# Optimization experiments

Hardware: AMD Instinct MI355X
Metric: run time of the kernel (lower is better)

Reference implementation:

```python
import jax, jax.numpy as jnp
import numpy as np

HEADS = 8
BN_EPS = 1e-5

def _bn(x2d, g, b):
    # torch BatchNorm1d in training mode: biased batch stats
    mu = x2d.mean(0)
    var = x2d.var(0)
    return (x2d - mu) * jax.lax.rsqrt(var + BN_EPS) * g + b

def _window_indices(H):
    # exclusive-end box coordinates, in the exact order of the torch loop
    m = H // 2
    r0, r1, c0, c1 = [], [], [], []
    for i in range(1, m + 1):
        wins = [(m - i, m + i + 1, m - i, m + i + 1),  # full square
                (m - i, m + 1,     m - i, m + i + 1),  # top half
                (m,     m + i + 1, m - i, m + i + 1),  # bottom half
                (m - i, m + i + 1, m - i, m + 1),      # left half
                (m - i, m + i + 1, m,     m + i + 1)]  # right half
        for a, b, c, d in wins:
            r0.append(a); r1.append(b); c0.append(c); c1.append(d)
    r0 = np.array(r0); r1 = np.array(r1); c0 = np.array(c0); c1 = np.array(c1)
    counts = ((r1 - r0) * (c1 - c0)).astype(np.float32)
    return r0, r1, c0, c1, counts

def _box_sums(P, r0, r1, c0, c1):
    # P: padded 2D prefix sum [B, C, H+1, H+1]; returns [B, C, K]
    return P[:, :, r1, c1] - P[:, :, r0, c1] - P[:, :, r1, c0] + P[:, :, r0, c0]

def _integral(img):
    return jnp.pad(jnp.cumsum(jnp.cumsum(img, axis=2), axis=3), ((0, 0), (0, 0), (1, 0), (1, 0)))

def setup_inputs() -> dict:
    key = jax.random.key(0)
    ks = jax.random.split(key, 8)
    B, Cin, H = 64, 512, 31
    C = 512  # heads * base_dim
    x = jax.random.normal(ks[0], (B, Cin, H, H), dtype=jnp.float32)
    w_v = jax.random.normal(ks[1], (Cin, C), dtype=jnp.float32) * 0.02
    w_k = jax.random.normal(ks[2], (Cin, C), dtype=jnp.float32) * 0.02
    w_fc = jax.random.normal(ks[3], (Cin + C, 512), dtype=jnp.float32) * 0.02
    z = lambda n: jnp.zeros((n,), jnp.float32)
    o = lambda n: jnp.ones((n,), jnp.float32)
    return {"x": x,
            "w_v": w_v, "b_v": z(C), "g_vn": o(C), "b_vn": z(C),
            "w_k": w_k, "b_k": z(C), "g_kn": o(C), "b_kn": z(C),
            "w_fc": w_fc, "b_fc": z(512), "g_fcn": o(512), "b_fcn": z(512)}

def reference(x, w_v, b_v, g_vn, b_vn, w_k, b_k, g_kn, b_kn, w_fc, b_fc, g_fcn, b_fcn):
    B, Cin, H, W = x.shape
    N = H * W
    C = w_v.shape[1]
    d = C // HEADS
    m = H // 2
    xt = x.reshape(B, Cin, N).transpose(0, 2, 1)       # [B, N, Cin]
    x0 = xt[:, N // 2, :]                              # [B, Cin] center pixel feature
    flat = xt.reshape(B * N, Cin)
    v = jax.nn.relu(_bn(flat @ w_v + b_v, g_vn, b_vn))
    v = v.reshape(B, N, C).transpose(0, 2, 1).reshape(B, C, H, H)
    k = _bn(flat @ w_k + b_k, g_kn, b_kn).reshape(B, N, HEADS, d).transpose(0, 2, 1, 3)  # [B,h,N,d]
    q = k[:, :, N // 2, :]                             # [B, h, d]
    attn = jax.nn.softmax(jnp.einsum('bhd,bhnd->bhn', q, k) * (d ** -0.5), axis=-1)      # [B,h,N]
    attn_full = jnp.broadcast_to(attn[:, :, None, :], (B, HEADS, d, N)).reshape(B, C, H, H)
    xw = attn_full * v                                 # attn-weighted values [B,C,H,H]
    eps = 1e-16
    r0, r1, c0, c1, counts = _window_indices(H)
    Px = _integral(xw)
    Pa = _integral(attn_full)
    mx = _box_sums(Px, r0, r1, c0, c1) / counts        # window means of xw   [B,C,K]
    ma = _box_sums(Pa, r0, r1, c0, c1) / counts        # window means of attn [B,C,K]
    y_win = (mx / (ma + eps)).transpose(0, 2, 1)       # [B, K, C]
    y = jnp.concatenate([xw[:, :, m, m][:, None, :], y_win], axis=1)  # [B, n, C]
    # F.normalize(p=2, dim=2)
    y = y / jnp.maximum(jnp.linalg.norm(y, axis=2, keepdims=True), 1e-12)
    n = y.shape[1]
    yy = jnp.concatenate([jnp.broadcast_to(x0[:, None, :], (B, n, Cin)), y], axis=-1)
    out = jax.nn.relu(_bn(yy.reshape(B * n, Cin + C) @ w_fc + b_fc, g_fcn, b_fcn))
    return out.reshape(B, n, -1)
```

## Files before the change

kernel.cpp:

```cpp
#include <hip/hip_runtime.h>
#include <stdint.h>

#define DEV __device__ __forceinline__

typedef __bf16 bf16x8 __attribute__((ext_vector_type(8)));
typedef unsigned short u16x8 __attribute__((ext_vector_type(8)));
typedef uint32_t u32x4 __attribute__((ext_vector_type(4)));
typedef float f32x4 __attribute__((ext_vector_type(4)));

#define NS 1024

DEV uint16_t f2bf(float f) {
    union { float f; uint32_t u; } v; v.f = f;
    uint32_t r = v.u + 0x7fffu + ((v.u >> 16) & 1u);
    return (uint16_t)(r >> 16);
}
DEV float bf2f(uint16_t h) {
    union { uint32_t u; float f; } v; v.u = ((uint32_t)h) << 16;
    return v.f;
}

#if __has_builtin(__builtin_amdgcn_cvt_pk_bf16_f32)
typedef __bf16 bf16x2 __attribute__((ext_vector_type(2)));
DEV uint32_t pk2bf(float lo, float hi) {
    bf16x2 r = __builtin_amdgcn_cvt_pk_bf16_f32(lo, hi);
    return __builtin_bit_cast(uint32_t, r);
}
#else
DEV uint32_t pk2bf(float lo, float hi) {
    return (uint32_t)f2bf(lo) | ((uint32_t)f2bf(hi) << 16);
}
#endif

DEV float scan32(float v, int lane) {
    #pragma unroll
    for (int d = 1; d < 32; d <<= 1) {
        float o = __shfl_up(v, d, 32);
        if (lane >= d) v += o;
    }
    return v;
}

DEV void win_idx(int w, int& r0, int& r1, int& c0, int& c1) {
    int i = w / 5 + 1, t = w % 5;
    const int m = 15;
    switch (t) {
        case 0: r0 = m - i; r1 = m + i + 1; c0 = m - i; c1 = m + i + 1; break;
        case 1: r0 = m - i; r1 = m + 1;     c0 = m - i; c1 = m + i + 1; break;
        case 2: r0 = m;     r1 = m + i + 1; c0 = m - i; c1 = m + i + 1; break;
        case 3: r0 = m - i; r1 = m + i + 1; c0 = m - i; c1 = m + 1;     break;
        default:r0 = m - i; r1 = m + i + 1; c0 = m;     c1 = m + i + 1; break;
    }
}

#if __has_builtin(__builtin_amdgcn_global_load_lds)
DEV void async16(const uint16_t* g, uint16_t* l) {
    __builtin_amdgcn_global_load_lds(
        (const __attribute__((address_space(1))) uint32_t*)g,
        (__attribute__((address_space(3))) uint32_t*)l, 16, 0, 0);
}
#else
DEV void async16(const uint16_t* g, uint16_t* l) {
    *(u16x8*)l = *(const u16x8*)g;
}
#endif

__global__ void k_convert_x(const float* __restrict__ x, uint16_t* __restrict__ xbt) {
    __shared__ float tile[32][33];
    int b = blockIdx.z;
    int n0 = blockIdx.x * 32;
    int c0 = blockIdx.y * 32;
    int tx = threadIdx.x, ty = threadIdx.y;
    #pragma unroll
    for (int i = 0; i < 4; ++i) {
        int c = c0 + ty + 8 * i;
        int n = n0 + tx;
        float v = 0.f;
        if (n < 961) v = x[((size_t)b * 512 + c) * 961 + n];
        tile[ty + 8 * i][tx] = v;
    }
    __syncthreads();
    int idx = ty * 32 + tx;
    int c4 = (idx & 7) * 4;
    int nl = idx >> 3;
    int n = n0 + nl;
    ushort4 val;
    val.x = f2bf(tile[c4 + 0][nl]);
    val.y = f2bf(tile[c4 + 1][nl]);
    val.z = f2bf(tile[c4 + 2][nl]);
    val.w = f2bf(tile[c4 + 3][nl]);
    *(ushort4*)&xbt[((size_t)b * NS + n) * 512 + c0 + c4] = val;
}

__global__ void k_convert_w(const float* __restrict__ wv, const float* __restrict__ wk,
                            const float* __restrict__ wfc,
                            uint16_t* __restrict__ wvkt, uint16_t* __restrict__ wfct,
                            uint16_t* __restrict__ wfrag) {
    int idx = blockIdx.x * 256 + threadIdx.x;
    if (idx < 524288) {
        int j = idx >> 9, k = idx & 511;
        float v = (j < 512) ? wv[(size_t)k * 512 + j] : wk[(size_t)k * 512 + (j - 512)];
        wvkt[idx] = f2bf(v);
    } else if (idx < 1048576) {
        int t = idx - 524288;
        int j = t >> 10, k = t & 1023;
        wfct[t] = f2bf(wfc[(size_t)k * 512 + j]);
    } else {
        int t = idx - 1048576;
        int e = t & 7;
        int lane = (t >> 3) & 63;
        int kt = (t >> 9) & 31;
        int mt = t >> 14;
        int m = mt * 16 + (lane & 15);
        int k = kt * 32 + (lane >> 4) * 8 + e;
        uint16_t out = 0;
        if (m < 75 && k < 961) {
            int r = k / 31, cc = k - r * 31;
            int r0, r1, c0, c1;
            win_idx(m, r0, r1, c0, c1);
            if (r >= r0 && r < r1 && cc >= c0 && cc < c1) out = 0x3f80;
        }
        wfrag[t] = out;
    }
}

template<int K, int EPI>
__global__ __launch_bounds__(256, 4)
void k_gemm(const uint16_t* __restrict__ A, const uint16_t* __restrict__ Bt,
            uint16_t* __restrict__ out_v, uint16_t* __restrict__ out_k,
            float* __restrict__ out_f,
            float* __restrict__ colsum, float* __restrict__ colsq)
{
    __shared__ __align__(16) uint16_t sbuf[16384];
    __shared__ float sStat[256];
    uint16_t* sA0 = sbuf;
    uint16_t* sA1 = sbuf + 4096;
    uint16_t* sB0 = sbuf + 8192;
    uint16_t* sB1 = sbuf + 12288;

    const int tid = threadIdx.x;
    const int wave = tid >> 6, lane = tid & 63;
    const int quad = lane >> 4, l16 = lane & 15;
    int m0, j0;
    if constexpr (EPI == 0) {
        int lin = blockIdx.x;
        int xcd = lin & 7, rest = lin >> 3;
        int jb = rest & 7, mhi = rest >> 3;
        m0 = (mhi * 8 + xcd) * 128; j0 = jb * 128;
    } else {
        m0 = blockIdx.y * 128; j0 = blockIdx.x * 128;
    }
    const int wm = wave >> 1, wj = wave & 1;

    const f32x4 fzero = {0.f, 0.f, 0.f, 0.f};
    f32x4 acc[4][4];
    #pragma unroll
    for (int i = 0; i < 4; ++i)
        #pragma unroll
        for (int j = 0; j < 4; ++j) acc[i][j] = fzero;

    const int c0 = tid;
    const int mA0 = c0 >> 2, kq0 = c0 & 3;
    const int c1 = tid + 256;
    const int mA1 = c1 >> 2, kq1 = c1 & 3;

    const int KT = K / 64;
    for (int kt = 0; kt < KT; ++kt) {
        const uint16_t* Ak = A + (size_t)m0 * K + kt * 64;
        const uint16_t* Bk = Bt + (size_t)j0 * K + kt * 64;
        async16(Ak + (size_t)mA0 * K + kq0 * 8,      &sA0[c0 * 8]);
        async16(Ak + (size_t)mA1 * K + kq1 * 8,      &sA0[c1 * 8]);
        async16(Ak + (size_t)mA0 * K + 32 + kq0 * 8, &sA1[c0 * 8]);
        async16(Ak + (size_t)mA1 * K + 32 + kq1 * 8, &sA1[c1 * 8]);
        async16(Bk + (size_t)mA0 * K + kq0 * 8,      &sB0[c0 * 8]);
        async16(Bk + (size_t)mA1 * K + kq1 * 8,      &sB0[c1 * 8]);
        async16(Bk + (size_t)mA0 * K + 32 + kq0 * 8, &sB1[c0 * 8]);
        async16(Bk + (size_t)mA1 * K + 32 + kq1 * 8, &sB1[c1 * 8]);
        __syncthreads();
        #pragma unroll
        for (int p = 0; p < 2; ++p) {
            const uint16_t* pA = p ? sA1 : sA0;
            const uint16_t* pB = p ? sB1 : sB0;
            bf16x8 af[4], bfr[4];
            #pragma unroll
            for (int i = 0; i < 4; ++i) {
                int m = wm * 64 + i * 16 + l16;
                u16x8 r = *(const u16x8*)&pA[m * 32 + quad * 8];
                af[i] = __builtin_bit_cast(bf16x8, r);
            }
            #pragma unroll
            for (int j = 0; j < 4; ++j) {
                int jj = wj * 64 + j * 16 + l16;
                u16x8 r = *(const u16x8*)&pB[jj * 32 + quad * 8];
                bfr[j] = __builtin_bit_cast(bf16x8, r);
            }
            #pragma unroll
            for (int i = 0; i < 4; ++i)
                #pragma unroll
                for (int j = 0; j < 4; ++j)
                    acc[i][j] = __builtin_amdgcn_mfma_f32_16x16x32_bf16(af[i], bfr[j], acc[i][j], 0, 0, 0);
        }
        __syncthreads();
    }

    sStat[tid] = 0.f;
    __syncthreads();

    #pragma unroll
    for (int j = 0; j < 4; ++j) {
        const int col_local = wj * 64 + j * 16 + l16;
        float ls = 0.f, lq = 0.f;
        #pragma unroll
        for (int i = 0; i < 4; ++i) {
            #pragma unroll
            for (int reg = 0; reg < 4; ++reg) {
                const float val = acc[i][j][reg];
                ls += val; lq += val * val;
                if constexpr (EPI == 1) {
                    const int r = m0 + wm * 64 + i * 16 + quad * 4 + reg;
                    out_f[(size_t)r * 512 + (j0 + col_local)] = val;
                }
            }
        }
        ls += __shfl_xor(ls, 16); lq += __shfl_xor(lq, 16);
        ls += __shfl_xor(ls, 32); lq += __shfl_xor(lq, 32);
        if (quad == 0) {
            atomicAdd(&sStat[col_local], ls);
            atomicAdd(&sStat[128 + col_local], lq);
        }
    }
    __syncthreads();
    if (tid < 128) atomicAdd(&colsum[j0 + tid], sStat[tid]);
    else           atomicAdd(&colsq[j0 + (tid & 127)], sStat[tid]);

    if constexpr (EPI == 0) {
        #pragma unroll
        for (int ch = 0; ch < 2; ++ch) {
            if (wj == ch) {
                #pragma unroll
                for (int j = 0; j < 4; ++j) {
                    const int c = j * 16 + l16;
                    #pragma unroll
                    for (int i = 0; i < 4; ++i) {
                        const int rloc = wm * 64 + i * 16 + quad * 4;
                        uint2 pp;
                        pp.x = pk2bf(acc[i][j][0], acc[i][j][1]);
                        pp.y = pk2bf(acc[i][j][2], acc[i][j][3]);
                        *(uint2*)&sbuf[c * 136 + rloc] = pp;
                    }
                }
            }
            __syncthreads();
            const int jg = j0 + ch * 64;
            uint16_t* const outp = (jg < 512) ? out_v : out_k;
            const int jbase = (jg < 512) ? jg : jg - 512;
            #pragma unroll
            for (int s = 0; s < 8; ++s) {
                const int chunk = tid + 256 * s;
                const int c = chunk >> 5, q = chunk & 31;
                uint2 val = *(const uint2*)&sbuf[c * 136 + q * 4];
                const int r = m0 + q * 4;
                const unsigned bb_ = (unsigned)r >> 10;
                const unsigned nn = (unsigned)r & 1023u;
                *(uint2*)&outp[((size_t)bb_ * 512 + jbase + c) * NS + nn] = val;
            }
            __syncthreads();
        }
    }
}

__global__ __launch_bounds__(256, 4)
void k_attnwin(const uint16_t* __restrict__ kraw, const uint16_t* __restrict__ vraw,
               const uint16_t* __restrict__ wfrag,
               const float* __restrict__ colsum, const float* __restrict__ colsq,
               const float* __restrict__ g_kn, const float* __restrict__ b_kn,
               const float* __restrict__ g_vn, const float* __restrict__ b_vn,
               float* __restrict__ y)
{
    __shared__ float qa[64];
    __shared__ float va[64], vb[64];
    __shared__ float atv[992];
    __shared__ __align__(16) uint16_t attb[1024];
    __shared__ float maw_s[80];
    __shared__ float cnt_s[80];
    __shared__ float red[4];
    __shared__ float s_qb, s_bmax, s_inv;

    const int bh = blockIdx.x;
    const int b = bh >> 3, h = bh & 7;
    const int tid = threadIdx.x;
    const int lane = tid & 63, wave = tid >> 6;
    const int quad = lane >> 4, l16 = lane & 15;
    constexpr float invM = 1.f / 61504.f;

    if (tid < 64) {
        int c = h * 64 + tid;
        float mean = colsum[512 + c] * invM;
        float q_ = colsq[512 + c] * invM;
        float a = g_kn[c] * rsqrtf(q_ - mean * mean + 1e-5f);
        float bb = b_kn[c] - mean * a;
        float kr = bf2f(kraw[((size_t)b * 512 + c) * NS + 480]);
        float qv = kr * a + bb;
        qa[tid] = qv * a;
        float qb = qv * bb;
        #pragma unroll
        for (int off = 32; off; off >>= 1) qb += __shfl_down(qb, off);
        if (tid == 0) s_qb = qb;
    } else if (tid < 128) {
        int t = tid - 64;
        int c = h * 64 + t;
        float mean = colsum[c] * invM;
        float q_ = colsq[c] * invM;
        float a = g_vn[c] * rsqrtf(q_ - mean * mean + 1e-5f);
        va[t] = a;
        vb[t] = b_vn[c] - mean * a;
    }
    __syncthreads();

    const int n4 = tid * 4;
    float lg[4];
    float lmax = -1e30f;
    {
        const uint16_t* kp = kraw + ((size_t)b * 512 + h * 64) * NS + n4;
        float a0 = 0.f, a1 = 0.f, a2 = 0.f, a3 = 0.f;
        if (n4 < 961) {
            #pragma unroll 16
            for (int dd = 0; dd < 64; ++dd) {
                uint2 kk = *(const uint2*)(kp + (size_t)dd * NS);
                u16x8 kk4 = {};
                kk4[0] = (uint16_t)(kk.x & 0xffffu);
                kk4[1] = (uint16_t)(kk.x >> 16);
                kk4[2] = (uint16_t)(kk.y & 0xffffu);
                kk4[3] = (uint16_t)(kk.y >> 16);
                float q = qa[dd];
                a0 += q * bf2f(kk4[0]);
                a1 += q * bf2f(kk4[1]);
                a2 += q * bf2f(kk4[2]);
                a3 += q * bf2f(kk4[3]);
            }
        }
        lg[0] = a0; lg[1] = a1; lg[2] = a2; lg[3] = a3;
        #pragma unroll
        for (int i = 0; i < 4; ++i) {
            lg[i] = (lg[i] + s_qb) * 0.125f;
            if (n4 + i < 961) lmax = fmaxf(lmax, lg[i]);
        }
    }
    #pragma unroll
    for (int off = 32; off; off >>= 1) lmax = fmaxf(lmax, __shfl_xor(lmax, off));
    if (lane == 0) red[wave] = lmax;
    __syncthreads();
    if (tid == 0) s_bmax = fmaxf(fmaxf(red[0], red[1]), fmaxf(red[2], red[3]));
    __syncthreads();
    float lsum = 0.f;
    #pragma unroll
    for (int i = 0; i < 4; ++i) {
        float e = (n4 + i < 961) ? __expf(lg[i] - s_bmax) : 0.f;
        lg[i] = e;
        lsum += e;
    }
    #pragma unroll
    for (int off = 32; off; off >>= 1) lsum += __shfl_xor(lsum, off);
    if (lane == 0) red[wave] = lsum;
    __syncthreads();
    if (tid == 0) s_inv = 1.f / (red[0] + red[1] + red[2] + red[3]);
    __syncthreads();
    {
        uint2 pk;
        float w0 = (n4 + 0 < 961) ? lg[0] * s_inv : 0.f;
        float w1 = (n4 + 1 < 961) ? lg[1] * s_inv : 0.f;
        float w2 = (n4 + 2 < 961) ? lg[2] * s_inv : 0.f;
        float w3 = (n4 + 3 < 961) ? lg[3] * s_inv : 0.f;
        pk.x = pk2bf(w0, w1);
        pk.y = pk2bf(w2, w3);
        *(uint2*)&attb[n4] = pk;
        #pragma unroll
        for (int i = 0; i < 4; ++i)
            if (n4 + i < 961) atv[n4 + i] = lg[i] * s_inv;
    }
    __syncthreads();

    if (tid < 64) {
        float vv = bf2f(vraw[((size_t)(b * 512 + h * 64 + tid)) * NS + 480]);
        y[(size_t)b * 76 * 512 + h * 64 + tid] = fmaxf(vv * va[tid] + vb[tid], 0.f) * atv[480];
    }
    __syncthreads();

    {
        int col = tid & 31, r8 = tid >> 5;
        #pragma unroll
        for (int p = 0; p < 4; ++p) {
            int row = p * 8 + r8;
            bool on = (row < 31) && (col < 31);
            float v = on ? atv[row * 31 + col] : 0.f;
            v = scan32(v, col);
            if (on) atv[row * 31 + col] = v;
        }
    }
    __syncthreads();
    {
        int r = tid & 31, c8 = tid >> 5;
        #pragma unroll
        for (int p = 0; p < 4; ++p) {
            int cc = p * 8 + c8;
            bool on = (cc < 31) && (r < 31);
            float v = on ? atv[r * 31 + cc] : 0.f;
            v = scan32(v, r);
            if (on) atv[r * 31 + cc] = v;
        }
    }
    __syncthreads();
    if (tid < 75) {
        int r0, r1, c0, c1;
        win_idx(tid, r0, r1, c0, c1);
        auto S = [&](int r, int c) -> float { return (r < 0 || c < 0) ? 0.f : atv[r * 31 + c]; };
        float box = S(r1 - 1, c1 - 1) - S(r0 - 1, c1 - 1) - S(r1 - 1, c0 - 1) + S(r0 - 1, c0 - 1);
        float cnt = (float)((r1 - r0) * (c1 - c0));
        cnt_s[tid] = cnt;
        maw_s[tid] = box / cnt;
    }
    __syncthreads();

    {
        const int cl = wave * 16 + l16;
        const float a_bn = va[cl], b_bn = vb[cl];
        const uint16_t* vp = vraw + ((size_t)(b * 512 + h * 64 + cl)) * NS + quad * 8;
        f32x4 acc5[5];
        const f32x4 fz = {0.f, 0.f, 0.f, 0.f};
        #pragma unroll
        for (int mt = 0; mt < 5; ++mt) acc5[mt] = fz;
        for (int kt = 0; kt < 31; ++kt) {
            u16x8 vv = *(const u16x8*)(vp + kt * 32);
            u16x8 aa = *(const u16x8*)&attb[kt * 32 + quad * 8];
            u32x4 bwu;
            #pragma unroll
            for (int e = 0; e < 4; ++e) {
                float x0 = fmaxf(bf2f(vv[2 * e]) * a_bn + b_bn, 0.f) * bf2f(aa[2 * e]);
                float x1 = fmaxf(bf2f(vv[2 * e + 1]) * a_bn + b_bn, 0.f) * bf2f(aa[2 * e + 1]);
                bwu[e] = pk2bf(x0, x1);
            }
            bf16x8 bfr = __builtin_bit_cast(bf16x8, bwu);
            #pragma unroll
            for (int mt = 0; mt < 5; ++mt) {
                u16x8 wf = *(const u16x8*)&wfrag[(((mt * 32 + kt) * 64 + lane)) * 8];
                acc5[mt] = __builtin_amdgcn_mfma_f32_16x16x32_bf16(
                    __builtin_bit_cast(bf16x8, wf), bfr, acc5[mt], 0, 0, 0);
            }
        }
        const int cg = h * 64 + cl;
        #pragma unroll
        for (int mt = 0; mt < 5; ++mt) {
            #pragma unroll
            for (int reg = 0; reg < 4; ++reg) {
                int w = mt * 16 + quad * 4 + reg;
                if (w < 75) {
                    float mx = acc5[mt][reg] / cnt_s[w];
                    y[((size_t)b * 76 + 1 + w) * 512 + cg] = mx / (maw_s[w] + 1e-16f);
                }
            }
        }
    }
}

__global__ void k_build_yy(const float* __restrict__ y, const uint16_t* __restrict__ xbt,
                           uint16_t* __restrict__ yy)
{
    __shared__ float red[4];
    int row = blockIdx.x;
    int b = row / 76;
    int tid = threadIdx.x;
    const float* yp = y + (size_t)row * 512;
    float v0 = yp[tid], v1 = yp[tid + 256];
    float ss = v0 * v0 + v1 * v1;
    for (int off = 32; off; off >>= 1) ss += __shfl_xor(ss, off);
    if ((tid & 63) == 0) red[tid >> 6] = ss;
    __syncthreads();
    float tot = red[0] + red[1] + red[2] + red[3];
    float inv = 1.f / fmaxf(sqrtf(tot), 1e-12f);
    uint16_t* op = yy + (size_t)row * 1024;
    const uint16_t* x0p = xbt + ((size_t)b * NS + 480) * 512;
    op[tid]           = x0p[tid];
    op[tid + 256]     = x0p[tid + 256];
    op[512 + tid]       = f2bf(v0 * inv);
    op[512 + tid + 256] = f2bf(v1 * inv);
}

__global__ void k_fcout(const float* __restrict__ fcraw,
                        const float* __restrict__ colsum, const float* __restrict__ colsq,
                        const float* __restrict__ g, const float* __restrict__ be,
                        float* __restrict__ out)
{
    size_t idx = (size_t)blockIdx.x * 256 + threadIdx.x;
    if (idx < (size_t)4864 * 512) {
        int j = (int)(idx & 511);
        constexpr float invM = 1.f / 4864.f;
        float mean = colsum[j] * invM;
        float q_ = colsq[j] * invM;
        float a = g[j] * rsqrtf(q_ - mean * mean + 1e-5f);
        float bb = be[j] - mean * a;
        out[idx] = fmaxf(fcraw[idx] * a + bb, 0.f);
    }
}

extern "C" void kernel_launch(void* const* d_in, const int* in_sizes, int n_in,
                              void* d_out, int out_size, void* d_ws, size_t ws_size,
                              hipStream_t stream)
{
    (void)in_sizes; (void)n_in; (void)out_size; (void)ws_size;
    const float* x    = (const float*)d_in[0];
    const float* w_v  = (const float*)d_in[1];
    const float* g_vn = (const float*)d_in[3];
    const float* b_vn = (const float*)d_in[4];
    const float* w_k  = (const float*)d_in[5];
    const float* g_kn = (const float*)d_in[7];
    const float* b_kn = (const float*)d_in[8];
    const float* w_fc = (const float*)d_in[9];
    const float* g_fcn = (const float*)d_in[11];
    const float* b_fcn = (const float*)d_in[12];
    float* out = (float*)d_out;

    char* base = (char*)d_ws;
    size_t off = 0;
    auto alloc = [&](size_t bytes) -> void* {
        void* p = base + off;
        off += (bytes + 255) & ~(size_t)255;
        return p;
    };
    uint16_t* xbt  = (uint16_t*)alloc((size_t)64 * NS * 512 * 2);
    uint16_t* wvkt = (uint16_t*)alloc((size_t)1024 * 512 * 2);
    uint16_t* wfct = (uint16_t*)alloc((size_t)512 * 1024 * 2);
    uint16_t* wfrag = (uint16_t*)alloc((size_t)5 * 32 * 64 * 8 * 2);
    uint16_t* vraw = (uint16_t*)alloc((size_t)64 * 512 * NS * 2);
    uint16_t* kraw = (uint16_t*)alloc((size_t)64 * 512 * NS * 2);
    float* stats   = (float*)alloc(3072 * 4);
    float* y       = (float*)alloc((size_t)64 * 76 * 512 * 4);
    uint16_t* yy   = (uint16_t*)alloc((size_t)4864 * 1024 * 2);
    float* fcraw   = (float*)alloc((size_t)4864 * 512 * 4);

    hipMemsetAsync(stats, 0, 3072 * 4, stream);
    k_convert_x<<<dim3(32, 16, 64), dim3(32, 8), 0, stream>>>(x, xbt);
    k_convert_w<<<4416, 256, 0, stream>>>(w_v, w_k, w_fc, wvkt, wfct, wfrag);

    k_gemm<512, 0><<<4096, 256, 0, stream>>>(xbt, wvkt, vraw, kraw, nullptr,
                                             stats, stats + 1024);

    k_attnwin<<<512, 256, 0, stream>>>(kraw, vraw, wfrag, stats, stats + 1024,
                                       g_kn, b_kn, g_vn, b_vn, y);
    k_build_yy<<<4864, 256, 0, stream>>>(y, xbt, yy);

    k_gemm<1024, 1><<<dim3(4, 38), 256, 0, stream>>>(yy, wfct, nullptr, nullptr, fcraw,
                                                     stats + 2048, stats + 2560);
    k_fcout<<<9728, 256, 0, stream>>>(fcraw, stats + 2048, stats + 2560, g_fcn, b_fcn, out);
}
```

Baseline: 423.6 us.

## Fuse fp32-to-bf16 transpose of x into the V/K projection GEMM A-load

Removes the separate k_convert_x kernel and its bf16 transposed copy of x. The QKV GEMM now reads fp32 x directly along the spatial dimension, converts to bf16 in registers and writes the transposed tile into padded LDS. This saves one full write and read pass of a 64x1024x512 bf16 buffer and one launch. The cost is a synchronous global load path in place of async LDS loads, and each wave reading 8 channel rows, which could lower load efficiency. build_yy now reads x0 from x directly.

```diff
diff --git a/kernel.cpp b/kernel.cpp
--- a/kernel.cpp
+++ b/kernel.cpp
@@ -64,33 +64,6 @@
     *(u16x8*)l = *(const u16x8*)g;
 }
 #endif
-
-__global__ void k_convert_x(const float* __restrict__ x, uint16_t* __restrict__ xbt) {
-    __shared__ float tile[32][33];
-    int b = blockIdx.z;
-    int n0 = blockIdx.x * 32;
-    int c0 = blockIdx.y * 32;
-    int tx = threadIdx.x, ty = threadIdx.y;
-    #pragma unroll
-    for (int i = 0; i < 4; ++i) {
-        int c = c0 + ty + 8 * i;
-        int n = n0 + tx;
-        float v = 0.f;
-        if (n < 961) v = x[((size_t)b * 512 + c) * 961 + n];
-        tile[ty + 8 * i][tx] = v;
-    }
-    __syncthreads();
-    int idx = ty * 32 + tx;
-    int c4 = (idx & 7) * 4;
-    int nl = idx >> 3;
-    int n = n0 + nl;
-    ushort4 val;
-    val.x = f2bf(tile[c4 + 0][nl]);
-    val.y = f2bf(tile[c4 + 1][nl]);
-    val.z = f2bf(tile[c4 + 2][nl]);
-    val.w = f2bf(tile[c4 + 3][nl]);
-    *(ushort4*)&xbt[((size_t)b * NS + n) * 512 + c0 + c4] = val;
-}
 
 __global__ void k_convert_w(const float* __restrict__ wv, const float* __restrict__ wk,
                             const float* __restrict__ wfc,
@@ -124,13 +97,156 @@
     }
 }
 
-template<int K, int EPI>
 __global__ __launch_bounds__(256, 4)
-void k_gemm(const uint16_t* __restrict__ A, const uint16_t* __restrict__ Bt,
-            uint16_t* __restrict__ out_v, uint16_t* __restrict__ out_k,
-            float* __restrict__ out_f,
-            float* __restrict__ colsum, float* __restrict__ colsq)
+void k_gemmx(const float* __restrict__ x, const uint16_t* __restrict__ Bt,
+             uint16_t* __restrict__ out_v, uint16_t* __restrict__ out_k,
+             float* __restrict__ colsum, float* __restrict__ colsq)
 {
+    constexpr int K = 512;
+    __shared__ __align__(16) uint16_t sA[2][128 * 40];
+    __shared__ __align__(16) uint16_t sB[2][128 * 32];
+    __shared__ float sStat[256];
+
+    const int tid = threadIdx.x;
+    const int wave = tid >> 6, lane = tid & 63;
+    const int quad = lane >> 4, l16 = lane & 15;
+    int lin = blockIdx.x;
+    int xcd = lin & 7, rest = lin >> 3;
+    int jb = rest & 7, mhi = rest >> 3;
+    const int mb = mhi * 8 + xcd;
+    const int m0 = mb * 128, j0 = jb * 128;
+    const int b = mb >> 3;
+    const int n0l = (mb & 7) * 128;
+    const bool full = (mb & 7) != 7;
+    const int wm = wave >> 1, wj = wave & 1;
+
+    const f32x4 fzero = {0.f, 0.f, 0.f, 0.f};
+    f32x4 acc[4][4];
+    #pragma unroll
+    for (int i = 0; i < 4; ++i)
+        #pragma unroll
+        for (int j = 0; j < 4; ++j) acc[i][j] = fzero;
+
+    const int c0 = tid, mA0 = c0 >> 2, kq0 = c0 & 3;
+    const int c1 = tid + 256, mA1 = c1 >> 2, kq1 = c1 & 3;
+
+    const bool ok1 = full || (n0l + 64 + lane) < 961;
+
+    for (int kt = 0; kt < 8; ++kt) {
+        const uint16_t* Bk = Bt + (size_t)j0 * K + kt * 64;
+        async16(Bk + (size_t)mA0 * K + kq0 * 8,      &sB[0][c0 * 8]);
+        async16(Bk + (size_t)mA1 * K + kq1 * 8,      &sB[0][c1 * 8]);
+        async16(Bk + (size_t)mA0 * K + 32 + kq0 * 8, &sB[1][c0 * 8]);
+        async16(Bk + (size_t)mA1 * K + 32 + kq1 * 8, &sB[1][c1 * 8]);
+        #pragma unroll
+        for (int p = 0; p < 2; ++p) {
+            const int cbase = kt * 64 + p * 32 + wave * 8;
+            const float* xc = x + (size_t)(b * 512 + cbase) * 961 + n0l + lane;
+            float v0[8], v1[8];
+            #pragma unroll
+            for (int cc = 0; cc < 8; ++cc) {
+                v0[cc] = xc[(size_t)cc * 961];
+                v1[cc] = ok1 ? xc[(size_t)cc * 961 + 64] : 0.f;
+            }
+            u32x4 w0, w1;
+            #pragma unroll
+            for (int g = 0; g < 4; ++g) {
+                w0[g] = pk2bf(v0[2 * g], v0[2 * g + 1]);
+                w1[g] = pk2bf(v1[2 * g], v1[2 * g + 1]);
+            }
+            *(u32x4*)&sA[p][lane * 40 + wave * 8]        = w0;
+            *(u32x4*)&sA[p][(64 + lane) * 40 + wave * 8] = w1;
+        }
+        __syncthreads();
+        #pragma unroll
+        for (int p = 0; p < 2; ++p) {
+            bf16x8 af[4], bfr[4];
+            #pragma unroll
+            for (int i = 0; i < 4; ++i) {
+                int m = wm * 64 + i * 16 + l16;
+                u16x8 r = *(const u16x8*)&sA[p][m * 40 + quad * 8];
+                af[i] = __builtin_bit_cast(bf16x8, r);
+            }
+            #pragma unroll
+            for (int j = 0; j < 4; ++j) {
+                int jj = wj * 64 + j * 16 + l16;
+                u16x8 r = *(const u16x8*)&sB[p][jj * 32 + quad * 8];
+                bfr[j] = __builtin_bit_cast(bf16x8, r);
+            }
+            #pragma unroll
+            for (int i = 0; i < 4; ++i)
+                #pragma unroll
+                for (int j = 0; j < 4; ++j)
+                    acc[i][j] = __builtin_amdgcn_mfma_f32_16x16x32_bf16(af[i], bfr[j], acc[i][j], 0, 0, 0);
+        }
+        __syncthreads();
+    }
+
+    sStat[tid] = 0.f;
+    __syncthreads();
+    #pragma unroll
+    for (int j = 0; j < 4; ++j) {
+        const int col_local = wj * 64 + j * 16 + l16;
+        float ls = 0.f, lq = 0.f;
+        #pragma unroll
+        for (int i = 0; i < 4; ++i)
+            #pragma unroll
+            for (int reg = 0; reg < 4; ++reg) {
+                const float val = acc[i][j][reg];
+                ls += val; lq += val * val;
+            }
+        ls += __shfl_xor(ls, 16); lq += __shfl_xor(lq, 16);
+        ls += __shfl_xor(ls, 32); lq += __shfl_xor(lq, 32);
+        if (quad == 0) {
+            atomicAdd(&sStat[col_local], ls);
+            atomicAdd(&sStat[128 + col_local], lq);
+        }
+    }
+    __syncthreads();
+    if (tid < 128) atomicAdd(&colsum[j0 + tid], sStat[tid]);
+    else           atomicAdd(&colsq[j0 + (tid & 127)], sStat[tid]);
+
+    uint16_t* tbuf = (uint16_t*)sA;
+    #pragma unroll
+    for (int ch = 0; ch < 2; ++ch) {
+        if (wj == ch) {
+            #pragma unroll
+            for (int j = 0; j < 4; ++j) {
+                const int c = j * 16 + l16;
+                #pragma unroll
+                for (int i = 0; i < 4; ++i) {
+                    const int rloc = wm * 64 + i * 16 + quad * 4;
+                    uint2 pp;
+                    pp.x = pk2bf(acc[i][j][0], acc[i][j][1]);
+                    pp.y = pk2bf(acc[i][j][2], acc[i][j][3]);
+                    *(uint2*)&tbuf[c * 136 + rloc] = pp;
+                }
+            }
+        }
+        __syncthreads();
+        const int jg = j0 + ch * 64;
+        uint16_t* const outp = (jg < 512) ? out_v : out_k;
+        const int jbase = (jg < 512) ? jg : jg - 512;
+        #pragma unroll
+        for (int s = 0; s < 8; ++s) {
+            const int chunk = tid + 256 * s;
+            const int c = chunk >> 5, q = chunk & 31;
+            uint2 val = *(const uint2*)&tbuf[c * 136 + q * 4];
+            const int r = m0 + q * 4;
+            const unsigned bb_ = (unsigned)r >> 10;
+            const unsigned nn = (unsigned)r & 1023u;
+            *(uint2*)&outp[((size_t)bb_ * 512 + jbase + c) * NS + nn] = val;
+        }
+        __syncthreads();
+    }
+}
+
+__global__ __launch_bounds__(256, 4)
+void k_gemm_fc(const uint16_t* __restrict__ A, const uint16_t* __restrict__ Bt,
+               float* __restrict__ out_f,
+               float* __restrict__ colsum, float* __restrict__ colsq)
+{
+    constexpr int K = 1024;
     __shared__ __align__(16) uint16_t sbuf[16384];
     __shared__ float sStat[256];
     uint16_t* sA0 = sbuf;
@@ -141,15 +257,7 @@
     const int tid = threadIdx.x;
     const int wave = tid >> 6, lane = tid & 63;
     const int quad = lane >> 4, l16 = lane & 15;
-    int m0, j0;
-    if constexpr (EPI == 0) {
-        int lin = blockIdx.x;
-        int xcd = lin & 7, rest = lin >> 3;
-        int jb = rest & 7, mhi = rest >> 3;
-        m0 = (mhi * 8 + xcd) * 128; j0 = jb * 128;
-    } else {
-        m0 = blockIdx.y * 128; j0 = blockIdx.x * 128;
-    }
+    const int m0 = blockIdx.y * 128, j0 = blockIdx.x * 128;
     const int wm = wave >> 1, wj = wave & 1;
 
     const f32x4 fzero = {0.f, 0.f, 0.f, 0.f};
@@ -159,13 +267,10 @@
         #pragma unroll
         for (int j = 0; j < 4; ++j) acc[i][j] = fzero;
 
-    const int c0 = tid;
-    const int mA0 = c0 >> 2, kq0 = c0 & 3;
-    const int c1 = tid + 256;
-    const int mA1 = c1 >> 2, kq1 = c1 & 3;
-
-    const int KT = K / 64;
-    for (int kt = 0; kt < KT; ++kt) {
+    const int c0 = tid, mA0 = c0 >> 2, kq0 = c0 & 3;
+    const int c1 = tid + 256, mA1 = c1 >> 2, kq1 = c1 & 3;
+
+    for (int kt = 0; kt < K / 64; ++kt) {
         const uint16_t* Ak = A + (size_t)m0 * K + kt * 64;
         const uint16_t* Bk = Bt + (size_t)j0 * K + kt * 64;
         async16(Ak + (size_t)mA0 * K + kq0 * 8,      &sA0[c0 * 8]);
@@ -205,7 +310,6 @@
 
     sStat[tid] = 0.f;
     __syncthreads();
-
     #pragma unroll
     for (int j = 0; j < 4; ++j) {
         const int col_local = wj * 64 + j * 16 + l16;
@@ -216,10 +320,8 @@
             for (int reg = 0; reg < 4; ++reg) {
                 const float val = acc[i][j][reg];
                 ls += val; lq += val * val;
-                if constexpr (EPI == 1) {
-                    const int r = m0 + wm * 64 + i * 16 + quad * 4 + reg;
-                    out_f[(size_t)r * 512 + (j0 + col_local)] = val;
-                }
+                const int r = m0 + wm * 64 + i * 16 + quad * 4 + reg;
+                out_f[(size_t)r * 512 + (j0 + col_local)] = val;
             }
         }
         ls += __shfl_xor(ls, 16); lq += __shfl_xor(lq, 16);
@@ -232,41 +334,6 @@
     __syncthreads();
     if (tid < 128) atomicAdd(&colsum[j0 + tid], sStat[tid]);
     else           atomicAdd(&colsq[j0 + (tid & 127)], sStat[tid]);
-
-    if constexpr (EPI == 0) {
-        #pragma unroll
-        for (int ch = 0; ch < 2; ++ch) {
-            if (wj == ch) {
-                #pragma unroll
-                for (int j = 0; j < 4; ++j) {
-                    const int c = j * 16 + l16;
-                    #pragma unroll
-                    for (int i = 0; i < 4; ++i) {
-                        const int rloc = wm * 64 + i * 16 + quad * 4;
-                        uint2 pp;
-                        pp.x = pk2bf(acc[i][j][0], acc[i][j][1]);
-                        pp.y = pk2bf(acc[i][j][2], acc[i][j][3]);
-                        *(uint2*)&sbuf[c * 136 + rloc] = pp;
-                    }
-                }
-            }
-            __syncthreads();
-            const int jg = j0 + ch * 64;
-            uint16_t* const outp = (jg < 512) ? out_v : out_k;
-            const int jbase = (jg < 512) ? jg : jg - 512;
-            #pragma unroll
-            for (int s = 0; s < 8; ++s) {
-                const int chunk = tid + 256 * s;
-                const int c = chunk >> 5, q = chunk & 31;
-                uint2 val = *(const uint2*)&sbuf[c * 136 + q * 4];
-                const int r = m0 + q * 4;
-                const unsigned bb_ = (unsigned)r >> 10;
-                const unsigned nn = (unsigned)r & 1023u;
-                *(uint2*)&outp[((size_t)bb_ * 512 + jbase + c) * NS + nn] = val;
-            }
-            __syncthreads();
-        }
-    }
 }
 
 __global__ __launch_bounds__(256, 4)
@@ -327,16 +394,11 @@
             #pragma unroll 16
             for (int dd = 0; dd < 64; ++dd) {
                 uint2 kk = *(const uint2*)(kp + (size_t)dd * NS);
-                u16x8 kk4 = {};
-                kk4[0] = (uint16_t)(kk.x & 0xffffu);
-                kk4[1] = (uint16_t)(kk.x >> 16);
-                kk4[2] = (uint16_t)(kk.y & 0xffffu);
-                kk4[3] = (uint16_t)(kk.y >> 16);
                 float q = qa[dd];
-                a0 += q * bf2f(kk4[0]);
-                a1 += q * bf2f(kk4[1]);
-                a2 += q * bf2f(kk4[2]);
-                a3 += q * bf2f(kk4[3]);
+                a0 += q * bf2f((uint16_t)(kk.x & 0xffffu));
+                a1 += q * bf2f((uint16_t)(kk.x >> 16));
+                a2 += q * bf2f((uint16_t)(kk.y & 0xffffu));
+                a3 += q * bf2f((uint16_t)(kk.y >> 16));
             }
         }
         lg[0] = a0; lg[1] = a1; lg[2] = a2; lg[3] = a3;
@@ -462,7 +524,7 @@
     }
 }
 
-__global__ void k_build_yy(const float* __restrict__ y, const uint16_t* __restrict__ xbt,
+__global__ void k_build_yy(const float* __restrict__ y, const float* __restrict__ x,
                            uint16_t* __restrict__ yy)
 {
     __shared__ float red[4];
@@ -478,9 +540,8 @@
     float tot = red[0] + red[1] + red[2] + red[3];
     float inv = 1.f / fmaxf(sqrtf(tot), 1e-12f);
     uint16_t* op = yy + (size_t)row * 1024;
-    const uint16_t* x0p = xbt + ((size_t)b * NS + 480) * 512;
-    op[tid]           = x0p[tid];
-    op[tid + 256]     = x0p[tid + 256];
+    op[tid]       = f2bf(x[(size_t)(b * 512 + tid) * 961 + 480]);
+    op[tid + 256] = f2bf(x[(size_t)(b * 512 + tid + 256) * 961 + 480]);
     op[512 + tid]       = f2bf(v0 * inv);
     op[512 + tid + 256] = f2bf(v1 * inv);
 }
@@ -526,7 +587,6 @@
         off += (bytes + 255) & ~(size_t)255;
         return p;
     };
-    uint16_t* xbt  = (uint16_t*)alloc((size_t)64 * NS * 512 * 2);
     uint16_t* wvkt = (uint16_t*)alloc((size_t)1024 * 512 * 2);
     uint16_t* wfct = (uint16_t*)alloc((size_t)512 * 1024 * 2);
     uint16_t* wfrag = (uint16_t*)alloc((size_t)5 * 32 * 64 * 8 * 2);
@@ -538,17 +598,15 @@
     float* fcraw   = (float*)alloc((size_t)4864 * 512 * 4);
 
     hipMemsetAsync(stats, 0, 3072 * 4, stream);
-    k_convert_x<<<dim3(32, 16, 64), dim3(32, 8), 0, stream>>>(x, xbt);
     k_convert_w<<<4416, 256, 0, stream>>>(w_v, w_k, w_fc, wvkt, wfct, wfrag);
 
-    k_gemm<512, 0><<<4096, 256, 0, stream>>>(xbt, wvkt, vraw, kraw, nullptr,
-                                             stats, stats + 1024);
+    k_gemmx<<<4096, 256, 0, stream>>>(x, wvkt, vraw, kraw, stats, stats + 1024);
 
     k_attnwin<<<512, 256, 0, stream>>>(kraw, vraw, wfrag, stats, stats + 1024,
                                        g_kn, b_kn, g_vn, b_vn, y);
-    k_build_yy<<<4864, 256, 0, stream>>>(y, xbt, yy);
-
-    k_gemm<1024, 1><<<dim3(4, 38), 256, 0, stream>>>(yy, wfct, nullptr, nullptr, fcraw,
-                                                     stats + 2048, stats + 2560);
+    k_build_yy<<<4864, 256, 0, stream>>>(y, x, yy);
+
+    k_gemm_fc<<<dim3(4, 38), 256, 0, stream>>>(yy, wfct, fcraw,
+                                               stats + 2048, stats + 2560);
     k_fcout<<<9728, 256, 0, stream>>>(fcraw, stats + 2048, stats + 2560, g_fcn, b_fcn, out);
 }
```

After: 438.6 us. +3.6%, slower.
